# Kernel optimization log

Hardware: AMD Instinct MI355X
Metric: run time of the kernel (lower is better)

Reference implementation:

```python
import jax, jax.numpy as jnp
import numpy as np

PH, PW = 7, 7  # pool_height, pool_width
B, H, W, C = 4, 56, 56, 256
R = 128  # number of ROIs


def setup_inputs() -> dict:
    key = jax.random.key(0)
    k1, k2, k3, k4, k5, k6 = jax.random.split(key, 6)
    features = jax.random.normal(k1, (B, H, W, C), dtype=jnp.float32)
    # ROIs: (batch_idx, y1, x1, y2, x2), inclusive corners, each side >= pool size
    bidx = jax.random.randint(k2, (R,), 0, B)
    y1 = jax.random.randint(k3, (R,), 0, H - PH)
    x1 = jax.random.randint(k4, (R,), 0, W - PW)
    hgt = jax.random.randint(k5, (R,), PH, H // 2 + PH)
    wid = jax.random.randint(k6, (R,), PW, W // 2 + PW)
    y2 = jnp.minimum(y1 + hgt - 1, H - 1)
    x2 = jnp.minimum(x1 + wid - 1, W - 1)
    rois = jnp.stack([bidx, y1, x1, y2, x2], axis=1).astype(jnp.int32)
    return {"features": features, "rois": rois}


def reference(features, rois):
    """ROI max-pooling: crop each ROI and adaptively max-pool into PHxPW bins.
    features: [B,H,W,C] float; rois: [R,5] int (batch, y1, x1, y2, x2) inclusive.
    Returns [R, PH, PW, C].
    """
    bidx, y1, x1, y2, x2 = (rois[:, i] for i in range(5))
    feats = features[bidx]                      # [R,H,W,C] gather per ROI
    rh = (y2 - y1 + 1)                          # [R] roi heights
    rw = (x2 - x1 + 1)                          # [R] roi widths
    hh = jnp.arange(H)
    ww = jnp.arange(W)
    off_h = hh[None, :] - y1[:, None]           # [R,H]
    off_w = ww[None, :] - x1[:, None]           # [R,W]
    in_h = (off_h >= 0) & (hh[None, :] <= y2[:, None])
    in_w = (off_w >= 0) & (ww[None, :] <= x2[:, None])
    # adaptive non-overlapping bin assignment: bin = floor(offset * P / roi_len)
    bin_h = jnp.clip((off_h * PH) // rh[:, None], 0, PH - 1)   # [R,H]
    bin_w = jnp.clip((off_w * PW) // rw[:, None], 0, PW - 1)   # [R,W]
    valid = in_h[:, :, None] & in_w[:, None, :]                 # [R,H,W]
    ridx = jnp.arange(R)[:, None, None]
    seg = ridx * (PH * PW) + bin_h[:, :, None] * PW + bin_w[:, None, :]
    seg = jnp.where(valid, seg, R * PH * PW)                    # dump invalid to extra slot
    data = feats.reshape(R * H * W, C)
    seg = seg.reshape(R * H * W)
    out = jax.ops.segment_max(data, seg, num_segments=R * PH * PW + 1)
    out = out[: R * PH * PW].reshape(R, PH, PW, C)
    return jnp.where(jnp.isfinite(out), out, 0.0)
```

## Files before the change

### kernel.cpp

```cpp
#include <hip/hip_runtime.h>
#include <math.h>

#define PH 7
#define PW 7
#define B_ 4
#define H_ 56
#define W_ 56
#define C_ 256
#define R_ 128

__global__ __launch_bounds__(64) void roi_pool_kernel(
    const float* __restrict__ feat,
    const int*   __restrict__ rois,
    float*       __restrict__ out)
{
    const int bin = blockIdx.x;
    const int r   = bin / (PH * PW);
    const int pp  = bin - r * (PH * PW);
    const int ph  = pp / PW;
    const int pw  = pp - ph * PW;

    const int b  = rois[r * 5 + 0];
    const int y1 = rois[r * 5 + 1];
    const int x1 = rois[r * 5 + 2];
    const int y2 = rois[r * 5 + 3];
    const int x2 = rois[r * 5 + 4];
    const int rh = y2 - y1 + 1;
    const int rw = x2 - x1 + 1;

    const int hs = y1 + (ph * rh + PH - 1) / PH;
    const int he = y1 + ((ph + 1) * rh + PH - 1) / PH - 1;
    const int ws = x1 + (pw * rw + PW - 1) / PW;
    const int we = x1 + ((pw + 1) * rw + PW - 1) / PW - 1;

    const int c0 = threadIdx.x * 4;
    const float* base = feat + ((size_t)b * H_ * W_) * C_ + c0;

    float4 m = make_float4(-INFINITY, -INFINITY, -INFINITY, -INFINITY);
    for (int y = hs; y <= he; ++y) {
        const float* rowp = base + (size_t)y * W_ * C_;
        for (int x = ws; x <= we; ++x) {
            const float4 v = *reinterpret_cast<const float4*>(rowp + (size_t)x * C_);
            m.x = fmaxf(m.x, v.x);
            m.y = fmaxf(m.y, v.y);
            m.z = fmaxf(m.z, v.z);
            m.w = fmaxf(m.w, v.w);
        }
    }

    if (hs > he || ws > we) m = make_float4(0.f, 0.f, 0.f, 0.f);

    *reinterpret_cast<float4*>(out + (size_t)bin * C_ + c0) = m;
}

extern "C" void kernel_launch(void* const* d_in, const int* in_sizes, int n_in,
                              void* d_out, int out_size, void* d_ws, size_t ws_size,
                              hipStream_t stream) {
    const float* feat = (const float*)d_in[0];
    const int*   rois = (const int*)d_in[1];
    float*       out  = (float*)d_out;

    const int nbins = R_ * PH * PW;
    roi_pool_kernel<<<nbins, 64, 0, stream>>>(feat, rois, out);
}
```

Before: 69.30 us.

## Split each bin's rows across two waves and reduce via shared memory

Each 256-thread block now handles two bins, and two waves split each bin's rows by parity. The partial maxima are combined through LDS after a barrier. The inner x loop is unrolled by two so more loads are in flight. The empty-bin zeroing is replaced by an isfinite check on the output. The goal is more memory-level parallelism per bin and more waves in flight. The cost is a block-wide barrier, LDS traffic and fewer blocks overall.

Measured after the change: 67.05 us. 3.2% less time.

```diff
diff --git a/kernel.cpp b/kernel.cpp
--- a/kernel.cpp
+++ b/kernel.cpp
@@ -9,16 +9,26 @@
 #define C_ 256
 #define R_ 128
 
-__global__ __launch_bounds__(64) void roi_pool_kernel(
+#define BINS_TOTAL (R_ * PH * PW)
+
+__global__ __launch_bounds__(256) void roi_pool_kernel(
     const float* __restrict__ feat,
     const int*   __restrict__ rois,
     float*       __restrict__ out)
 {
-    const int bin = blockIdx.x;
-    const int r   = bin / (PH * PW);
-    const int pp  = bin - r * (PH * PW);
-    const int ph  = pp / PW;
-    const int pw  = pp - ph * PW;
+    __shared__ float4 red[2][64];
+
+    const int tid      = threadIdx.x;
+    const int wave     = tid >> 6;
+    const int lane     = tid & 63;
+    const int binLocal = wave >> 1;
+    const int sub      = wave & 1;
+    const int bin      = blockIdx.x * 2 + binLocal;
+
+    const int r  = bin / (PH * PW);
+    const int pp = bin - r * (PH * PW);
+    const int ph = pp / PW;
+    const int pw = pp - ph * PW;
 
     const int b  = rois[r * 5 + 0];
     const int y1 = rois[r * 5 + 1];
@@ -33,13 +43,23 @@
     const int ws = x1 + (pw * rw + PW - 1) / PW;
     const int we = x1 + ((pw + 1) * rw + PW - 1) / PW - 1;
 
-    const int c0 = threadIdx.x * 4;
+    const int c0 = lane * 4;
     const float* base = feat + ((size_t)b * H_ * W_) * C_ + c0;
 
     float4 m = make_float4(-INFINITY, -INFINITY, -INFINITY, -INFINITY);
-    for (int y = hs; y <= he; ++y) {
+
+    for (int y = hs + sub; y <= he; y += 2) {
         const float* rowp = base + (size_t)y * W_ * C_;
-        for (int x = ws; x <= we; ++x) {
+        int x = ws;
+        for (; x + 1 <= we; x += 2) {
+            const float4 v0 = *reinterpret_cast<const float4*>(rowp + (size_t)x * C_);
+            const float4 v1 = *reinterpret_cast<const float4*>(rowp + (size_t)(x + 1) * C_);
+            m.x = fmaxf(m.x, fmaxf(v0.x, v1.x));
+            m.y = fmaxf(m.y, fmaxf(v0.y, v1.y));
+            m.z = fmaxf(m.z, fmaxf(v0.z, v1.z));
+            m.w = fmaxf(m.w, fmaxf(v0.w, v1.w));
+        }
+        if (x <= we) {
             const float4 v = *reinterpret_cast<const float4*>(rowp + (size_t)x * C_);
             m.x = fmaxf(m.x, v.x);
             m.y = fmaxf(m.y, v.y);
@@ -48,9 +68,20 @@
         }
     }
 
-    if (hs > he || ws > we) m = make_float4(0.f, 0.f, 0.f, 0.f);
-
-    *reinterpret_cast<float4*>(out + (size_t)bin * C_ + c0) = m;
+    if (sub) red[binLocal][lane] = m;
+    __syncthreads();
+    if (!sub) {
+        const float4 o = red[binLocal][lane];
+        m.x = fmaxf(m.x, o.x);
+        m.y = fmaxf(m.y, o.y);
+        m.z = fmaxf(m.z, o.z);
+        m.w = fmaxf(m.w, o.w);
+        m.x = isfinite(m.x) ? m.x : 0.f;
+        m.y = isfinite(m.y) ? m.y : 0.f;
+        m.z = isfinite(m.z) ? m.z : 0.f;
+        m.w = isfinite(m.w) ? m.w : 0.f;
+        *reinterpret_cast<float4*>(out + (size_t)bin * C_ + c0) = m;
+    }
 }
 
 extern "C" void kernel_launch(void* const* d_in, const int* in_sizes, int n_in,
@@ -60,6 +91,5 @@
     const int*   rois = (const int*)d_in[1];
     float*       out  = (float*)d_out;
 
-    const int nbins = R_ * PH * PW;
-    roi_pool_kernel<<<nbins, 64, 0, stream>>>(feat, rois, out);
+    roi_pool_kernel<<<BINS_TOTAL / 2, 256, 0, stream>>>(feat, rois, out);
 }
```
